# Performance work log

Hardware: AMD Instinct MI355X
Metric: run time of the kernel (lower is better)

Reference implementation:

```python
import jax, jax.numpy as jnp
import numpy as np

B, N, HIST, D, E, NH = 1024, 2, 64, 256, 128, 8
HD = D // NH


def _linear_params(key, fan_in, fan_out):
    kw, kb = jax.random.split(key)
    lim = 1.0 / np.sqrt(fan_in)
    W = jax.random.uniform(kw, (fan_in, fan_out), jnp.float32, -lim, lim)
    b = jax.random.uniform(kb, (fan_out,), jnp.float32, -lim, lim)
    return W, b


def setup_inputs() -> dict:
    key = jax.random.key(0)
    ks = jax.random.split(key, 11)
    inp = {
        "node_features": jax.random.normal(ks[0], (B, N, HIST, D), jnp.float32),
        "edge_features": jax.random.normal(ks[1], (B, E), jnp.float32),
    }
    inp["Wq"], inp["bq"] = _linear_params(ks[2], D, D)
    inp["Wk"], inp["bk"] = _linear_params(ks[3], D, D)
    inp["Wv"], inp["bv"] = _linear_params(ks[4], D, D)
    inp["Wo"], inp["bo"] = _linear_params(ks[5], D, D)
    inp["Wbias"], inp["bbias"] = _linear_params(ks[6], E, NH)
    inp["Wgate"], inp["bgate"] = _linear_params(ks[7], E, D)
    inp["Wscale"], inp["bscale"] = _linear_params(ks[8], E, D)
    inp["Wshift"], inp["bshift"] = _linear_params(ks[9], E, D)
    inp["Whead"], inp["bhead"] = _linear_params(ks[10], E, NH)
    return inp


def reference(node_features, edge_features, Wq, bq, Wk, bk, Wv, bv, Wo, bo,
              Wbias, bbias, Wgate, bgate, Wscale, bscale, Wshift, bshift,
              Whead, bhead) -> jnp.ndarray:
    b, n, hist, d = node_features.shape
    s = n * hist  # seq_len (temporal mode)
    x = node_features.reshape(b, s, d)

    Q = x @ Wq + bq
    K = x @ Wk + bk
    V = x @ Wv + bv

    # Edge-conditioned modulation of V (ECC-style gate/scale/shift)
    gate = jax.nn.sigmoid(edge_features @ Wgate + bgate)      # [b, d]
    scale = jnp.tanh(edge_features @ Wscale + bscale)         # [b, d]
    shift = edge_features @ Wshift + bshift                   # [b, d]
    V = (V * (1.0 + scale[:, None, :]) + shift[:, None, :]) * gate[:, None, :]

    # [b, nh, s, hd]
    Q = Q.reshape(b, s, NH, HD).transpose(0, 2, 1, 3)
    K = K.reshape(b, s, NH, HD).transpose(0, 2, 1, 3)
    V = V.reshape(b, s, NH, HD).transpose(0, 2, 1, 3)

    scores = jnp.einsum('bhqd,bhkd->bhqk', Q, K) * (1.0 / np.sqrt(HD))

    edge_bias = edge_features @ Wbias + bbias                 # [b, nh]
    head_scale = jnp.tanh(edge_features @ Whead + bhead)      # [b, nh]
    scores = scores * (1.0 + head_scale[:, :, None, None])

    # attention bias: edge_bias placed at (t, hist+t) and (hist+t, t)
    t = jnp.arange(hist)
    eb = jnp.broadcast_to(edge_bias[:, :, None], (b, NH, hist))
    attention_bias = jnp.zeros((b, NH, s, s), scores.dtype)
    attention_bias = attention_bias.at[:, :, t, hist + t].set(eb)
    attention_bias = attention_bias.at[:, :, hist + t, t].set(eb)

    attn = jax.nn.softmax(scores + attention_bias, axis=-1)   # dropout in eval mode = identity
    out = jnp.einsum('bhqk,bhkd->bhqd', attn, V)
    out = out.transpose(0, 2, 1, 3).reshape(b, n, hist, d)
    out = out[:, :, -1, :]                                    # last timestep per node
    return out @ Wo + bo
```

## Files before the change

### kernel.cpp

```cpp
#include <hip/hip_runtime.h>
#include <cstdint>
#include <cstddef>


typedef short bf16x8 __attribute__((ext_vector_type(8)));
typedef float f32x4 __attribute__((ext_vector_type(4)));

#define MFMA16(A, B, C) __builtin_amdgcn_mfma_f32_16x16x32_bf16((A), (B), (C), 0, 0, 0)

static __device__ __forceinline__ uint16_t f2bf(float f) {
    uint32_t u = __builtin_bit_cast(uint32_t, f);
    u += 0x7FFFu + ((u >> 16) & 1u);
    return (uint16_t)(u >> 16);
}
static __device__ __forceinline__ uint32_t pack2(float a, float b) {
    return (uint32_t)f2bf(a) | ((uint32_t)f2bf(b) << 16);
}

__global__ __launch_bounds__(256) void k_wt(
    const float* __restrict__ Wq, const float* __restrict__ Wv,
    const float* __restrict__ Wo, const float* __restrict__ Wk,
    uint16_t* __restrict__ WqT, uint16_t* __restrict__ WvT,
    uint16_t* __restrict__ WoT, uint16_t* __restrict__ WkB)
{
    const int t = threadIdx.x;
    const int tr = blockIdx.x, tc = blockIdx.y, z = blockIdx.z;
    if (z == 3) {
        #pragma unroll
        for (int i = 0; i < 16; i++) {
            int flat = i * 256 + t;
            int lr = flat >> 6, lc = flat & 63;
            WkB[(size_t)(tr * 64 + lr) * 264 + tc * 64 + lc] =
                f2bf(Wk[(size_t)(tr * 64 + lr) * 256 + tc * 64 + lc]);
        }
        return;
    }
    const float* W = (z == 0) ? Wq : ((z == 1) ? Wv : Wo);
    uint16_t* O = (z == 0) ? WqT : ((z == 1) ? WvT : WoT);
    __shared__ float tile[64][65];
    #pragma unroll
    for (int i = 0; i < 16; i++) {
        int flat = i * 256 + t;
        int lr = flat >> 6, lc = flat & 63;
        tile[lr][lc] = W[(size_t)(tr * 64 + lr) * 256 + tc * 64 + lc];
    }
    __syncthreads();
    #pragma unroll
    for (int i = 0; i < 16; i++) {
        int flat = i * 256 + t;
        int orow = flat >> 6, oc = flat & 63;
        O[(size_t)(tc * 64 + orow) * 264 + tr * 64 + oc] = f2bf(tile[oc][orow]);
    }
}

__global__ __launch_bounds__(256) void k_edge(
    const float* __restrict__ edge,
    const float* __restrict__ Wgate, const float* __restrict__ bgate,
    const float* __restrict__ Wscale, const float* __restrict__ bscale,
    const float* __restrict__ Wshift, const float* __restrict__ bshift,
    const float* __restrict__ Wbias, const float* __restrict__ bbias,
    const float* __restrict__ Whead, const float* __restrict__ bhead,
    float* __restrict__ sp, float* __restrict__ tp, float* __restrict__ ebhs)
{
    __shared__ float eL[512];
    const int t = threadIdx.x;
    const int b0 = blockIdx.x * 4;
    for (int idx = t; idx < 512; idx += 256) {
        int bi = idx >> 7, e = idx & 127;
        eL[bi * 128 + e] = edge[(size_t)(b0 + bi) * 128 + e];
    }
    __syncthreads();
    float ag[4] = {0, 0, 0, 0}, asr[4] = {0, 0, 0, 0}, ah[4] = {0, 0, 0, 0};
    for (int e = 0; e < 128; e++) {
        float wg = Wgate[e * 256 + t];
        float wsc = Wscale[e * 256 + t];
        float wsh = Wshift[e * 256 + t];
        #pragma unroll
        for (int bi = 0; bi < 4; bi++) {
            float xv = eL[bi * 128 + e];
            ag[bi] = fmaf(xv, wg, ag[bi]);
            asr[bi] = fmaf(xv, wsc, asr[bi]);
            ah[bi] = fmaf(xv, wsh, ah[bi]);
        }
    }
    float bg = bgate[t], bs = bscale[t], bsh = bshift[t];
    #pragma unroll
    for (int bi = 0; bi < 4; bi++) {
        float g = 1.0f / (1.0f + __expf(-(ag[bi] + bg)));
        float sc = tanhf(asr[bi] + bs);
        float sh = ah[bi] + bsh;
        sp[(size_t)(b0 + bi) * 256 + t] = (1.0f + sc) * g;
        tp[(size_t)(b0 + bi) * 256 + t] = sh * g;
    }
    if (t < 64) {
        int bi = t >> 4, o = t & 15, h = o & 7;
        const float* W = (o < 8) ? Wbias : Whead;
        float a = 0.0f;
        for (int e = 0; e < 128; e++) a = fmaf(eL[bi * 128 + e], W[e * 8 + h], a);
        float val = (o < 8) ? (a + bbias[h]) : tanhf(a + bhead[h]);
        ebhs[(size_t)(b0 + bi) * 16 + o] = val;
    }
}

__global__ __launch_bounds__(256) void k_qu(
    const float* __restrict__ node, const uint16_t* __restrict__ WqT,
    const uint16_t* __restrict__ WkB, const float* __restrict__ bq,
    uint16_t* __restrict__ U)
{
    __shared__ uint16_t xq[16 * 264];
    __shared__ uint16_t QL[16 * 264];
    const int t = threadIdx.x, lane = t & 63, w = t >> 6, c = lane & 15, quad = lane >> 4;
    const int b0 = blockIdx.x * 4;
    #pragma unroll
    for (int i = 0; i < 4; i++) {
        int flat4 = i * 256 + t;
        int row = flat4 >> 6, c4 = flat4 & 63;
        int r = row & 7;
        int bb = b0 + (r >> 1);
        int s = (r & 1) ? 127 : 63;
        const float4 v = *(const float4*)(node + ((size_t)(bb * 128 + s)) * 256 + c4 * 4);
        uint2 pv; pv.x = pack2(v.x, v.y); pv.y = pack2(v.z, v.w);
        *(uint2*)&xq[row * 264 + c4 * 4] = pv;
    }
    __syncthreads();
    f32x4 zero = {0, 0, 0, 0};
    f32x4 acc[4];
    #pragma unroll
    for (int i = 0; i < 4; i++) acc[i] = zero;
    #pragma unroll
    for (int kk = 0; kk < 8; kk++) {
        bf16x8 afr = *(const bf16x8*)&xq[c * 264 + kk * 32 + quad * 8];
        #pragma unroll
        for (int i = 0; i < 4; i++) {
            int nt = w * 4 + i;
            bf16x8 bfr = *(const bf16x8*)&WqT[(size_t)(nt * 16 + c) * 264 + kk * 32 + quad * 8];
            acc[i] = MFMA16(afr, bfr, acc[i]);
        }
    }
    #pragma unroll
    for (int i = 0; i < 4; i++) {
        int nt = w * 4 + i;
        float bqv = bq[nt * 16 + c];
        #pragma unroll
        for (int r = 0; r < 4; r++) {
            QL[(quad * 4 + r) * 264 + nt * 16 + c] = f2bf(acc[i][r] + bqv);
        }
    }
    __syncthreads();
    for (int hh = 0; hh < 8; hh++) {
        bf16x8 bfr = *(const bf16x8*)&QL[c * 264 + hh * 32 + quad * 8];
        #pragma unroll
        for (int i = 0; i < 4; i++) {
            int mt = w * 4 + i;
            bf16x8 afr = *(const bf16x8*)&WkB[(size_t)(mt * 16 + c) * 264 + hh * 32 + quad * 8];
            f32x4 d = MFMA16(afr, bfr, zero);
            if (c < 8) {
                int bb = b0 + (c >> 1);
                int qh = (c & 1) * 8 + hh;
                uint2 pk; pk.x = pack2(d[0], d[1]); pk.y = pack2(d[2], d[3]);
                *(uint2*)&U[((size_t)(bb * 16 + qh)) * 256 + mt * 16 + quad * 4] = pk;
            }
        }
    }
}

__global__ __launch_bounds__(256, 2) void k_main(
    const float* __restrict__ node,
    const uint16_t* __restrict__ U,
    const float* __restrict__ ebhs,
    uint16_t* __restrict__ Y)
{
    __shared__ uint16_t xc[64 * 264];
    __shared__ uint16_t uL[16 * 264];
    __shared__ uint16_t pL[16 * 72];
    __shared__ float wred[2][16][4];
    __shared__ float stM[16], stL[16], stA[16];
    __shared__ float ebhsL[16];
    const int b = blockIdx.x;
    const int t = threadIdx.x, lane = t & 63, w = t >> 6, c = lane & 15, quad = lane >> 4;
    #pragma unroll
    for (int i = 0; i < 2; i++) {
        int flat = i * 256 + t;
        int row = flat >> 5, c16 = flat & 31;
        uint4 v = *(const uint4*)&U[((size_t)b * 16 + row) * 256 + c16 * 8];
        *(uint4*)&uL[row * 264 + c16 * 8] = v;
    }
    if (t < 16) { ebhsL[t] = ebhs[(size_t)b * 16 + t]; stM[t] = -1e30f; stL[t] = 0.0f; }
    __syncthreads();
    const int q = c >> 3, h = c & 7;
    const float scaleF = 0.17677669529663687f * (1.0f + ebhsL[8 + h]);
    const float ebv = ebhsL[h];
    f32x4 zero = {0, 0, 0, 0};
    f32x4 yacc[4];
    #pragma unroll
    for (int tt = 0; tt < 4; tt++) yacc[tt] = zero;

    for (int ch = 0; ch < 2; ch++) {
        #pragma unroll
        for (int i = 0; i < 16; i++) {
            int flat4 = i * 256 + t;
            int row = flat4 >> 6, c4 = flat4 & 63;
            const float4 v = *(const float4*)(node + ((size_t)b * 128 + ch * 64 + row) * 256 + c4 * 4);
            uint2 pv; pv.x = pack2(v.x, v.y); pv.y = pack2(v.z, v.w);
            *(uint2*)&xc[row * 264 + c4 * 4] = pv;
        }
        __syncthreads();
        f32x4 sacc = zero;
        #pragma unroll
        for (int kk = 0; kk < 8; kk++) {
            bf16x8 afr = *(const bf16x8*)&xc[(w * 16 + c) * 264 + kk * 32 + quad * 8];
            bf16x8 bfr = *(const bf16x8*)&uL[c * 264 + kk * 32 + quad * 8];
            sacc = MFMA16(afr, bfr, sacc);
        }
        float v0[4];
        #pragma unroll
        for (int r = 0; r < 4; r++) {
            int krow = ch * 64 + w * 16 + quad * 4 + r;
            float x = sacc[r] * scaleF;
            if ((q == 0 && krow == 127) || (q == 1 && krow == 63)) x += ebv;
            v0[r] = x;
        }
        float lmax = fmaxf(fmaxf(v0[0], v0[1]), fmaxf(v0[2], v0[3]));
        lmax = fmaxf(lmax, __shfl_xor(lmax, 16, 64));
        lmax = fmaxf(lmax, __shfl_xor(lmax, 32, 64));
        if (lane < 16) wred[0][c][w] = lmax;
        __syncthreads();
        float cmax = fmaxf(fmaxf(wred[0][c][0], wred[0][c][1]), fmaxf(wred[0][c][2], wred[0][c][3]));
        float mold = stM[c];
        float mnew = fmaxf(mold, cmax);
        float alpha = __expf(mold - mnew);
        float p0[4]; float lsum = 0.0f;
        #pragma unroll
        for (int r = 0; r < 4; r++) { p0[r] = __expf(v0[r] - mnew); lsum += p0[r]; }
        lsum += __shfl_xor(lsum, 16, 64);
        lsum += __shfl_xor(lsum, 32, 64);
        if (lane < 16) wred[1][c][w] = lsum;
        __syncthreads();
        if (w == 0 && lane < 16) {
            float csum = wred[1][c][0] + wred[1][c][1] + wred[1][c][2] + wred[1][c][3];
            stL[c] = stL[c] * alpha + csum;
            stM[c] = mnew;
            stA[c] = alpha;
        }
        {
            uint2 pk; pk.x = pack2(p0[0], p0[1]); pk.y = pack2(p0[2], p0[3]);
            *(uint2*)&pL[c * 72 + w * 16 + quad * 4] = pk;
        }
        __syncthreads();
        float av[4];
        #pragma unroll
        for (int r = 0; r < 4; r++) av[r] = stA[quad * 4 + r];
        #pragma unroll
        for (int tt = 0; tt < 4; tt++)
            #pragma unroll
            for (int r = 0; r < 4; r++) yacc[tt][r] *= av[r];
        #pragma unroll
        for (int kk = 0; kk < 2; kk++) {
            bf16x8 afr = *(const bf16x8*)&pL[c * 72 + kk * 32 + quad * 8];
            int kbase = kk * 32 + quad * 8;
            #pragma unroll
            for (int tt = 0; tt < 4; tt++) {
                int n = w * 64 + tt * 16 + c;
                union { bf16x8 v; uint32_t u[4]; } bb;
                #pragma unroll
                for (int jj = 0; jj < 4; jj++) {
                    uint32_t lo = xc[(kbase + 2 * jj) * 264 + n];
                    uint32_t hi = xc[(kbase + 2 * jj + 1) * 264 + n];
                    bb.u[jj] = lo | (hi << 16);
                }
                yacc[tt] = MFMA16(afr, bb.v, yacc[tt]);
            }
        }
        __syncthreads();
    }
    float invl[4];
    #pragma unroll
    for (int r = 0; r < 4; r++) invl[r] = 1.0f / stL[quad * 4 + r];
    #pragma unroll
    for (int tt = 0; tt < 4; tt++) {
        int n = w * 64 + tt * 16 + c;
        #pragma unroll
        for (int r = 0; r < 4; r++) {
            int qh = quad * 4 + r;
            int hq = qh & 7, qq = qh >> 3;
            Y[((size_t)(hq * 2048 + b * 2 + qq)) * 256 + n] = f2bf(yacc[tt][r] * invl[r]);
        }
    }
}

__global__ __launch_bounds__(256) void k_out(
    const uint16_t* __restrict__ Y,
    const uint16_t* __restrict__ WvT, const uint16_t* __restrict__ WoT,
    const float* __restrict__ bv, const float* __restrict__ bo,
    const float* __restrict__ sp, const float* __restrict__ tp,
    float* __restrict__ out)
{
    __shared__ uint16_t yh[2 * 16 * 264];
    __shared__ uint16_t zm[16 * 264];
    const int t = threadIdx.x, lane = t & 63, w = t >> 6, c = lane & 15, quad = lane >> 4;
    const int R0 = blockIdx.x * 16;
    f32x4 zero = {0, 0, 0, 0};
    for (int hp = 0; hp < 4; hp++) {
        __syncthreads();
        #pragma unroll
        for (int i = 0; i < 4; i++) {
            int flat = i * 256 + t;
            int hl = flat >> 9, rem = flat & 511;
            int row = rem >> 5, c16 = rem & 31;
            uint4 v = *(const uint4*)&Y[((size_t)((2 * hp + hl) * 2048 + R0 + row)) * 256 + c16 * 8];
            *(uint4*)&yh[(hl * 16 + row) * 264 + c16 * 8] = v;
        }
        __syncthreads();
        int hl = w >> 1, nt = w & 1;
        int h = 2 * hp + hl;
        f32x4 zacc = zero;
        #pragma unroll
        for (int kk = 0; kk < 8; kk++) {
            bf16x8 afr = *(const bf16x8*)&yh[(hl * 16 + c) * 264 + kk * 32 + quad * 8];
            bf16x8 bfr = *(const bf16x8*)&WvT[(size_t)(h * 32 + nt * 16 + c) * 264 + kk * 32 + quad * 8];
            zacc = MFMA16(afr, bfr, zacc);
        }
        int col = h * 32 + nt * 16 + c;
        float bvv = bv[col];
        #pragma unroll
        for (int r = 0; r < 4; r++) {
            int row = quad * 4 + r;
            int b = (R0 + row) >> 1;
            float z = zacc[r] + bvv;
            zm[row * 264 + col] = f2bf(z * sp[(size_t)b * 256 + col] + tp[(size_t)b * 256 + col]);
        }
    }
    __syncthreads();
    #pragma unroll
    for (int i = 0; i < 4; i++) {
        int nt = w * 4 + i;
        int n = nt * 16 + c;
        f32x4 fa = zero;
        #pragma unroll
        for (int kk = 0; kk < 8; kk++) {
            bf16x8 afr = *(const bf16x8*)&zm[c * 264 + kk * 32 + quad * 8];
            bf16x8 bfr = *(const bf16x8*)&WoT[(size_t)n * 264 + kk * 32 + quad * 8];
            fa = MFMA16(afr, bfr, fa);
        }
        float bov = bo[n];
        #pragma unroll
        for (int r = 0; r < 4; r++) {
            out[(size_t)(R0 + quad * 4 + r) * 256 + n] = fa[r] + bov;
        }
    }
}

extern "C" void kernel_launch(void* const* d_in, const int* in_sizes, int n_in,
                              void* d_out, int out_size, void* d_ws, size_t ws_size,
                              hipStream_t stream) {
    const float* node   = (const float*)d_in[0];
    const float* edge   = (const float*)d_in[1];
    const float* Wq     = (const float*)d_in[2];
    const float* bq     = (const float*)d_in[3];
    const float* Wk     = (const float*)d_in[4];
    const float* Wv     = (const float*)d_in[6];
    const float* bv     = (const float*)d_in[7];
    const float* Wo     = (const float*)d_in[8];
    const float* bo     = (const float*)d_in[9];
    const float* Wbias  = (const float*)d_in[10];
    const float* bbias  = (const float*)d_in[11];
    const float* Wgate  = (const float*)d_in[12];
    const float* bgate  = (const float*)d_in[13];
    const float* Wscale = (const float*)d_in[14];
    const float* bscale = (const float*)d_in[15];
    const float* Wshift = (const float*)d_in[16];
    const float* bshift = (const float*)d_in[17];
    const float* Whead  = (const float*)d_in[18];
    const float* bhead  = (const float*)d_in[19];

    char* ws = (char*)d_ws;
    uint16_t* WqT  = (uint16_t*)(ws + 0);
    uint16_t* WvT  = (uint16_t*)(ws + 135168);
    uint16_t* WoT  = (uint16_t*)(ws + 270336);
    uint16_t* WkB  = (uint16_t*)(ws + 405504);
    float*    spw  = (float*)(ws + 540672);
    float*    tpw  = (float*)(ws + 1589248);
    float*    ebhs = (float*)(ws + 2637824);
    uint16_t* Uw   = (uint16_t*)(ws + 2703360);
    uint16_t* Yw   = (uint16_t*)(ws + 11091968);

    k_wt<<<dim3(4, 4, 4), 256, 0, stream>>>(Wq, Wv, Wo, Wk, WqT, WvT, WoT, WkB);
    k_edge<<<256, 256, 0, stream>>>(edge, Wgate, bgate, Wscale, bscale, Wshift, bshift,
                                    Wbias, bbias, Whead, bhead, spw, tpw, ebhs);
    k_qu<<<256, 256, 0, stream>>>(node, WqT, WkB, bq, Uw);
    k_main<<<1024, 256, 0, stream>>>(node, Uw, ebhs, Yw);
    k_out<<<128, 256, 0, stream>>>(Yw, WvT, WoT, bv, bo, spw, tpw, (float*)d_out);
}
```

Before: 289.9 us.

## Merge weight-prep and edge kernels, swizzle node LDS tile, raise main occupancy

```diff
diff --git a/kernel.cpp b/kernel.cpp
--- a/kernel.cpp
+++ b/kernel.cpp
@@ -17,43 +17,11 @@
     return (uint32_t)f2bf(a) | ((uint32_t)f2bf(b) << 16);
 }
 
-__global__ __launch_bounds__(256) void k_wt(
+__global__ __launch_bounds__(256) void k_prep(
     const float* __restrict__ Wq, const float* __restrict__ Wv,
     const float* __restrict__ Wo, const float* __restrict__ Wk,
     uint16_t* __restrict__ WqT, uint16_t* __restrict__ WvT,
-    uint16_t* __restrict__ WoT, uint16_t* __restrict__ WkB)
-{
-    const int t = threadIdx.x;
-    const int tr = blockIdx.x, tc = blockIdx.y, z = blockIdx.z;
-    if (z == 3) {
-        #pragma unroll
-        for (int i = 0; i < 16; i++) {
-            int flat = i * 256 + t;
-            int lr = flat >> 6, lc = flat & 63;
-            WkB[(size_t)(tr * 64 + lr) * 264 + tc * 64 + lc] =
-                f2bf(Wk[(size_t)(tr * 64 + lr) * 256 + tc * 64 + lc]);
-        }
-        return;
-    }
-    const float* W = (z == 0) ? Wq : ((z == 1) ? Wv : Wo);
-    uint16_t* O = (z == 0) ? WqT : ((z == 1) ? WvT : WoT);
-    __shared__ float tile[64][65];
-    #pragma unroll
-    for (int i = 0; i < 16; i++) {
-        int flat = i * 256 + t;
-        int lr = flat >> 6, lc = flat & 63;
-        tile[lr][lc] = W[(size_t)(tr * 64 + lr) * 256 + tc * 64 + lc];
-    }
-    __syncthreads();
-    #pragma unroll
-    for (int i = 0; i < 16; i++) {
-        int flat = i * 256 + t;
-        int orow = flat >> 6, oc = flat & 63;
-        O[(size_t)(tc * 64 + orow) * 264 + tr * 64 + oc] = f2bf(tile[oc][orow]);
-    }
-}
-
-__global__ __launch_bounds__(256) void k_edge(
+    uint16_t* __restrict__ WoT, uint16_t* __restrict__ WkB,
     const float* __restrict__ edge,
     const float* __restrict__ Wgate, const float* __restrict__ bgate,
     const float* __restrict__ Wscale, const float* __restrict__ bscale,
@@ -62,9 +30,41 @@
     const float* __restrict__ Whead, const float* __restrict__ bhead,
     float* __restrict__ sp, float* __restrict__ tp, float* __restrict__ ebhs)
 {
-    __shared__ float eL[512];
+    __shared__ float smem[64 * 65];
     const int t = threadIdx.x;
-    const int b0 = blockIdx.x * 4;
+    const int bid = blockIdx.x;
+    if (bid < 64) {
+        const int z = bid >> 4, tr = (bid >> 2) & 3, tc = bid & 3;
+        if (z == 3) {
+            #pragma unroll
+            for (int i = 0; i < 16; i++) {
+                int flat = i * 256 + t;
+                int lr = flat >> 6, lc = flat & 63;
+                WkB[(size_t)(tr * 64 + lr) * 264 + tc * 64 + lc] =
+                    f2bf(Wk[(size_t)(tr * 64 + lr) * 256 + tc * 64 + lc]);
+            }
+            return;
+        }
+        const float* W = (z == 0) ? Wq : ((z == 1) ? Wv : Wo);
+        uint16_t* O = (z == 0) ? WqT : ((z == 1) ? WvT : WoT);
+        float (*tile)[65] = (float (*)[65])smem;
+        #pragma unroll
+        for (int i = 0; i < 16; i++) {
+            int flat = i * 256 + t;
+            int lr = flat >> 6, lc = flat & 63;
+            tile[lr][lc] = W[(size_t)(tr * 64 + lr) * 256 + tc * 64 + lc];
+        }
+        __syncthreads();
+        #pragma unroll
+        for (int i = 0; i < 16; i++) {
+            int flat = i * 256 + t;
+            int orow = flat >> 6, oc = flat & 63;
+            O[(size_t)(tc * 64 + orow) * 264 + tr * 64 + oc] = f2bf(tile[oc][orow]);
+        }
+        return;
+    }
+    float* eL = smem;
+    const int b0 = (bid - 64) * 4;
     for (int idx = t; idx < 512; idx += 256) {
         int bi = idx >> 7, e = idx & 127;
         eL[bi * 128 + e] = edge[(size_t)(b0 + bi) * 128 + e];
@@ -164,7 +164,7 @@
     }
 }
 
-__global__ __launch_bounds__(256, 2) void k_main(
+__global__ __launch_bounds__(256, 3) void k_main(
     const float* __restrict__ node,
     const uint16_t* __restrict__ U,
     const float* __restrict__ ebhs,
@@ -202,15 +202,21 @@
             int row = flat4 >> 6, c4 = flat4 & 63;
             const float4 v = *(const float4*)(node + ((size_t)b * 128 + ch * 64 + row) * 256 + c4 * 4);
             uint2 pv; pv.x = pack2(v.x, v.y); pv.y = pack2(v.z, v.w);
-            *(uint2*)&xc[row * 264 + c4 * 4] = pv;
+            int col = (c4 * 4 + ((row >> 3) & 3) * 16) & 255;
+            *(uint2*)&xc[row * 264 + col] = pv;
         }
         __syncthreads();
         f32x4 sacc = zero;
-        #pragma unroll
-        for (int kk = 0; kk < 8; kk++) {
-            bf16x8 afr = *(const bf16x8*)&xc[(w * 16 + c) * 264 + kk * 32 + quad * 8];
-            bf16x8 bfr = *(const bf16x8*)&uL[c * 264 + kk * 32 + quad * 8];
-            sacc = MFMA16(afr, bfr, sacc);
+        {
+            int arow = w * 16 + c;
+            int sh = ((arow >> 3) & 3) * 16;
+            #pragma unroll
+            for (int kk = 0; kk < 8; kk++) {
+                int colA = (kk * 32 + quad * 8 + sh) & 255;
+                bf16x8 afr = *(const bf16x8*)&xc[arow * 264 + colA];
+                bf16x8 bfr = *(const bf16x8*)&uL[c * 264 + kk * 32 + quad * 8];
+                sacc = MFMA16(afr, bfr, sacc);
+            }
         }
         float v0[4];
         #pragma unroll
@@ -258,14 +264,16 @@
         for (int kk = 0; kk < 2; kk++) {
             bf16x8 afr = *(const bf16x8*)&pL[c * 72 + kk * 32 + quad * 8];
             int kbase = kk * 32 + quad * 8;
+            int sh = ((kbase >> 3) & 3) * 16;
             #pragma unroll
             for (int tt = 0; tt < 4; tt++) {
                 int n = w * 64 + tt * 16 + c;
+                int col = (n + sh) & 255;
                 union { bf16x8 v; uint32_t u[4]; } bb;
                 #pragma unroll
                 for (int jj = 0; jj < 4; jj++) {
-                    uint32_t lo = xc[(kbase + 2 * jj) * 264 + n];
-                    uint32_t hi = xc[(kbase + 2 * jj + 1) * 264 + n];
+                    uint32_t lo = xc[(kbase + 2 * jj) * 264 + col];
+                    uint32_t hi = xc[(kbase + 2 * jj + 1) * 264 + col];
                     bb.u[jj] = lo | (hi << 16);
                 }
                 yacc[tt] = MFMA16(afr, bb.v, yacc[tt]);
@@ -384,8 +392,8 @@
     uint16_t* Uw   = (uint16_t*)(ws + 2703360);
     uint16_t* Yw   = (uint16_t*)(ws + 11091968);
 
-    k_wt<<<dim3(4, 4, 4), 256, 0, stream>>>(Wq, Wv, Wo, Wk, WqT, WvT, WoT, WkB);
-    k_edge<<<256, 256, 0, stream>>>(edge, Wgate, bgate, Wscale, bscale, Wshift, bshift,
+    k_prep<<<320, 256, 0, stream>>>(Wq, Wv, Wo, Wk, WqT, WvT, WoT, WkB,
+                                    edge, Wgate, bgate, Wscale, bscale, Wshift, bshift,
                                     Wbias, bbias, Whead, bhead, spw, tpw, ebhs);
     k_qu<<<256, 256, 0, stream>>>(node, WqT, WkB, bq, Uw);
     k_main<<<1024, 256, 0, stream>>>(node, Uw, ebhs, Yw);
```

Result: no change. 286.7 us (-1.1%).
